# Kernel optimization log

Hardware: AMD Instinct MI355X
Metric: run time of the kernel (lower is better)

The kernel has to match this reference:

```python
import jax, jax.numpy as jnp
import numpy as np

HEADS = 12
HEAD_SIZE = 64
INF = 1e12  # K.infinity() in bert4keras

B, L, D = 8, 1024, 768


def setup_inputs() -> dict:
    key = jax.random.key(0)
    k1, k2 = jax.random.split(key)
    x = jax.random.normal(k1, (B, L, D), dtype=jnp.float32)
    W = jax.random.normal(k2, (D, HEADS * HEAD_SIZE * 2), dtype=jnp.float32) * (1.0 / np.sqrt(D))
    b = jnp.zeros((HEADS * HEAD_SIZE * 2,), dtype=jnp.float32)
    mask = jnp.ones((B, L), dtype=jnp.int32)
    return {"x": x, "W": W, "b": b, "mask": mask}


def _rope_sin_cos(seq_len, head_size, dtype):
    # SinusoidalPositionEmbedding(head_size, 'zero'):
    # emb[n, 2i] = sin(n * 10000^(-2i/S)), emb[n, 2i+1] = cos(...)
    pos = jnp.arange(seq_len, dtype=dtype)                       # [L]
    inv = jnp.power(jnp.asarray(10000.0, dtype),
                    -2.0 * jnp.arange(head_size // 2, dtype=dtype) / head_size)  # [S/2]
    ang = pos[:, None] * inv[None, :]                            # [L, S/2]
    # repeat_elements(..., 2, -1): [c0,c0,c1,c1,...]
    cos_pos = jnp.repeat(jnp.cos(ang), 2, axis=-1)               # [L, S]
    sin_pos = jnp.repeat(jnp.sin(ang), 2, axis=-1)               # [L, S]
    return sin_pos[None, :, None, :], cos_pos[None, :, None, :]  # [1,L,1,S]


def _rotate_half_interleaved(t):
    # stack([-t[...,1::2], t[...,::2]], -1).reshape(t.shape)
    t2 = jnp.stack([-t[..., 1::2], t[..., ::2]], axis=-1)
    return t2.reshape(t.shape)


def reference(x, W, b, mask):
    dtype = x.dtype
    Bq, Lq, _ = x.shape
    S = HEAD_SIZE
    # dense projection + head split: [B, L, H, 2S]
    proj = (jnp.einsum('bld,de->ble', x, W) + b).reshape(Bq, Lq, HEADS, 2 * S)
    qw, kw = proj[..., :S], proj[..., S:]
    # inline RoPE (interleaved variant)
    sin_pos, cos_pos = _rope_sin_cos(Lq, S, dtype)
    qw = qw * cos_pos + _rotate_half_interleaved(qw) * sin_pos
    kw = kw * cos_pos + _rotate_half_interleaved(kw) * sin_pos
    # bilinear score: [B, H, L, L]
    logits = jnp.einsum('bmhd,bnhd->bhmn', qw, kw)
    # padding mask on axis 2 (rows) and axis 3 (cols): x*m + (-INF)*(1-m)
    m = mask.astype(dtype)
    m_row = m[:, None, :, None]
    m_col = m[:, None, None, :]
    logits = logits * m_row + (-INF) * (1.0 - m_row)
    logits = logits * m_col + (-INF) * (1.0 - m_col)
    # upper-triangular (incl. diagonal) mask
    tri = jnp.triu(jnp.ones((Lq, Lq), dtype=dtype))
    logits = logits - (1.0 - tri) * INF
    return logits / np.sqrt(S).astype(np.float32)
```

## Files before the change

### kernel.cpp

```cpp
#include <hip/hip_runtime.h>
#include <hip/hip_bf16.h>
#include <stdint.h>

#define NHEADS 12
#define HS 64
#define NB 8
#define NL 1024
#define ND 768
#define NE 1536
#define INFV 1000000000000.0f

typedef __bf16 bf16x8 __attribute__((ext_vector_type(8)));
typedef float f32x4 __attribute__((ext_vector_type(4)));

typedef __attribute__((address_space(1))) const unsigned int gas_uint;
typedef __attribute__((address_space(3))) unsigned int las_uint;
#define GLOAD_LDS16(g, l) __builtin_amdgcn_global_load_lds((gas_uint*)(g), (las_uint*)(l), 16, 0, 0)

__device__ __forceinline__ unsigned short f2bf(float f) {
  unsigned int u = __builtin_bit_cast(unsigned int, f);
  u += 0x7fffu + ((u >> 16) & 1u);
  return (unsigned short)(u >> 16);
}

__device__ __forceinline__ bf16x8 load_frag(const unsigned short* p) {
  uint4 v = *(const uint4*)p;
  return __builtin_bit_cast(bf16x8, v);
}

__global__ __launch_bounds__(256) void k_prep(
    const float* __restrict__ W,
    unsigned short* __restrict__ wt,
    float* __restrict__ cst) {
  const int blk = blockIdx.x;
  if (blk < 288) {
    __shared__ float tile[64][65];
    int te = blk % 24, td = blk / 24;
    int c = threadIdx.x & 63, r4 = threadIdx.x >> 6;
    #pragma unroll
    for (int rr = 0; rr < 16; rr++) {
      int row = rr * 4 + r4;
      tile[row][c] = W[(size_t)(td * 64 + row) * NE + te * 64 + c];
    }
    __syncthreads();
    #pragma unroll
    for (int rr = 0; rr < 16; rr++) {
      int row = rr * 4 + r4;
      wt[(size_t)(te * 64 + row) * ND + td * 64 + c] = f2bf(tile[c][row]);
    }
  } else {
    int t = (blk - 288) * 256 + threadIdx.x;
    int p = t >> 5, i = t & 31;
    float inv = powf(10000.0f, -(float)i / 32.0f);
    float sv, cv;
    sincosf((float)p * inv, &sv, &cv);
    cst[(p * 32 + i) * 2 + 0] = cv;
    cst[(p * 32 + i) * 2 + 1] = sv;
  }
}

__global__ __launch_bounds__(256) void k_proj_rope(
    const float* __restrict__ x,
    const unsigned short* __restrict__ wt,
    const float* __restrict__ bias,
    const float* __restrict__ cst,
    unsigned short* __restrict__ qbuf, unsigned short* __restrict__ kbuf) {
  const int blk = blockIdx.x;
  const int xcd = blk & 7;
  const int loc = blk >> 3;
  const int h   = loc % 12;
  const int mt  = xcd * 8 + loc / 12;
  const int m0  = mt * 128;
  const int e0  = h * 128;
  const int tid  = threadIdx.x;
  const int lane = tid & 63;
  const int w    = tid >> 6;
  const int wm = w >> 1, wn = w & 1;
  const int col_l = lane & 15, rq = lane >> 4;

  __shared__ char smem_b[49152];

  unsigned int goffA[4];
  #pragma unroll
  for (int q = 0; q < 4; q++) {
    int p = q * 256 + tid;
    int r = p >> 3, sl = p & 7;
    goffA[q] = r * ND + (sl ^ (r & 7)) * 8;
  }
  unsigned int goffB[8];
  #pragma unroll
  for (int q = 0; q < 8; q++) {
    int p = q * 256 + tid;
    int r = p >> 4, sl = p & 15;
    goffB[q] = r * ND + (sl ^ (r & 15)) * 4;
  }
  const unsigned short* gA = wt + (size_t)e0 * ND;
  const float*          gB = x  + (size_t)m0 * ND;

  const int xr = col_l & 7;
  const unsigned int aRow = (unsigned)((wn * 64 + col_l) * 128);
  const unsigned int bRow = (unsigned)(16384 + (wm * 64 + col_l) * 256);

  f32x4 acc[4][4];
  #pragma unroll
  for (int i = 0; i < 4; i++)
    #pragma unroll
    for (int j = 0; j < 4; j++)
      #pragma unroll
      for (int q = 0; q < 4; q++) acc[i][j][q] = 0.0f;

  for (int kk = 0; kk < ND; kk += 64) {
    const unsigned short* sA = gA + kk;
    const float*          sB = gB + kk;
    #pragma unroll
    for (int q = 0; q < 4; q++) GLOAD_LDS16(sA + goffA[q], smem_b + (q * 256 + tid) * 16);
    #pragma unroll
    for (int q = 0; q < 8; q++) GLOAD_LDS16(sB + goffB[q], smem_b + 16384 + (q * 256 + tid) * 16);
    __syncthreads();
    #pragma unroll
    for (int kkh = 0; kkh < 2; kkh++) {
      bf16x8 af[4], bfr[4];
      #pragma unroll
      for (int f = 0; f < 4; f++) {
        af[f] = __builtin_bit_cast(bf16x8,
            *(const uint4*)(smem_b + aRow + f * 2048 + (((kkh << 2) | rq) ^ xr) * 16));
        const int sl0 = (kkh << 3) | (rq << 1);
        float4 lo = *(const float4*)(smem_b + bRow + f * 4096 + ((sl0 ^ col_l) * 16));
        float4 hi = *(const float4*)(smem_b + bRow + f * 4096 + (((sl0 + 1) ^ col_l) * 16));
        bfr[f] = bf16x8{(__bf16)lo.x, (__bf16)lo.y, (__bf16)lo.z, (__bf16)lo.w,
                        (__bf16)hi.x, (__bf16)hi.y, (__bf16)hi.z, (__bf16)hi.w};
      }
      #pragma unroll
      for (int i = 0; i < 4; i++)
        #pragma unroll
        for (int j = 0; j < 4; j++)
          acc[i][j] = __builtin_amdgcn_mfma_f32_16x16x32_bf16(af[i], bfr[j], acc[i][j], 0, 0, 0);
    }
    __syncthreads();
  }

  unsigned short* obuf = (wn == 1) ? kbuf : qbuf;
  #pragma unroll
  for (int j = 0; j < 4; j++) {
    const int m   = m0 + wm * 64 + j * 16 + col_l;
    const int pos = m & (NL - 1);
    const int bb  = m >> 10;
    const float* crow = cst + pos * 64;
    unsigned short* orow = obuf + (((size_t)(bb * NHEADS + h)) * NL + pos) * HS;
    #pragma unroll
    for (int i = 0; i < 4; i++) {
      const int s0 = i * 16 + rq * 4;
      float4 bv = *(const float4*)&bias[e0 + wn * 64 + s0];
      float4 tq = *(const float4*)(crow + s0);
      float v0 = acc[i][j][0] + bv.x;
      float v1 = acc[i][j][1] + bv.y;
      float v2 = acc[i][j][2] + bv.z;
      float v3 = acc[i][j][3] + bv.w;
      ushort4 o;
      o.x = f2bf(v0 * tq.x - v1 * tq.y);
      o.y = f2bf(v1 * tq.x + v0 * tq.y);
      o.z = f2bf(v2 * tq.z - v3 * tq.w);
      o.w = f2bf(v3 * tq.z + v2 * tq.w);
      *(ushort4*)&orow[s0] = o;
    }
  }
}

__global__ __launch_bounds__(256) void k_logits(
    const unsigned short* __restrict__ qbuf,
    const unsigned short* __restrict__ kbuf,
    const int* __restrict__ mask,
    float* __restrict__ out) {
  const int f  = blockIdx.x;
  const int r  = f & 7, t = f >> 3;
  const int bh = r + 8 * (t >> 6);
  const int tile = t & 63;
  const int tm = tile >> 3, tn = tile & 7;
  const int b  = bh / NHEADS;
  const int tid  = threadIdx.x;
  const int* mrow = mask + b * NL;

  if (tn < tm) {
    const int n0 = tn * 128 + (tid & 31) * 4;
    int4 mc = *(const int4*)&mrow[n0];
    #pragma unroll
    for (int it = 0; it < 16; it++) {
      int m = tm * 128 + it * 8 + (tid >> 5);
      float mr = (float)mrow[m];
      float base = -INFV * (1.0f - mr);
      f32x4 o;
      o[0] = ((mc.x ? base : -INFV) - INFV) * 0.125f;
      o[1] = ((mc.y ? base : -INFV) - INFV) * 0.125f;
      o[2] = ((mc.z ? base : -INFV) - INFV) * 0.125f;
      o[3] = ((mc.w ? base : -INFV) - INFV) * 0.125f;
      __builtin_nontemporal_store(o, (f32x4*)(out + ((size_t)bh * NL + m) * NL + n0));
    }
    return;
  }

  const int lane = tid & 63;
  const int w    = tid >> 6;
  const int wm = w >> 1, wn = w & 1;
  const int m_base = tm * 128 + wm * 64;
  const int n_base = tn * 128 + wn * 64;
  const int col_l = lane & 15, rq = lane >> 4;
  const unsigned short* Q = qbuf + (size_t)bh * (NL * HS);
  const unsigned short* K = kbuf + (size_t)bh * (NL * HS);

  __shared__ float lds[64 * 132];

  f32x4 acc[4][4];
  #pragma unroll
  for (int i = 0; i < 4; i++)
    #pragma unroll
    for (int j = 0; j < 4; j++)
      #pragma unroll
      for (int q = 0; q < 4; q++) acc[i][j][q] = 0.0f;

  #pragma unroll
  for (int ks = 0; ks < 2; ks++) {
    bf16x8 ak[4], bq[4];
    #pragma unroll
    for (int ff = 0; ff < 4; ff++) {
      ak[ff] = load_frag(K + (size_t)(n_base + ff * 16 + col_l) * HS + ks * 32 + rq * 8);
      bq[ff] = load_frag(Q + (size_t)(m_base + ff * 16 + col_l) * HS + ks * 32 + rq * 8);
    }
    #pragma unroll
    for (int i = 0; i < 4; i++)
      #pragma unroll
      for (int j = 0; j < 4; j++)
        acc[i][j] = __builtin_amdgcn_mfma_f32_16x16x32_bf16(ak[i], bq[j], acc[i][j], 0, 0, 0);
  }

  const bool diag = (tn == tm);
  const int rb_row = tid >> 5;
  const int rb_c4  = (tid & 31) * 4;
  const int n_rb   = tn * 128 + rb_c4;
  int4 mc_rb = *(const int4*)&mrow[n_rb];
  const bool allmc = (mc_rb.x & mc_rb.y & mc_rb.z & mc_rb.w) != 0;

  #pragma unroll
  for (int pass = 0; pass < 2; pass++) {
    if (wm == pass) {
      #pragma unroll
      for (int j = 0; j < 4; j++) {
        const int rl = j * 16 + col_l;
        #pragma unroll
        for (int i = 0; i < 4; i++)
          *(f32x4*)&lds[rl * 132 + wn * 64 + i * 16 + rq * 4] = acc[i][j];
      }
    }
    __syncthreads();
    #pragma unroll
    for (int it = 0; it < 8; it++) {
      const int rl = it * 8 + rb_row;
      const int m  = tm * 128 + pass * 64 + rl;
      f32x4 v = *(const f32x4*)&lds[rl * 132 + rb_c4];
      if (mrow[m] == 0) { v[0] = -INFV; v[1] = -INFV; v[2] = -INFV; v[3] = -INFV; }
      if (!allmc) {
        if (mc_rb.x == 0) v[0] = -INFV;
        if (mc_rb.y == 0) v[1] = -INFV;
        if (mc_rb.z == 0) v[2] = -INFV;
        if (mc_rb.w == 0) v[3] = -INFV;
      }
      if (diag) {
        if (n_rb + 0 < m) v[0] -= INFV;
        if (n_rb + 1 < m) v[1] -= INFV;
        if (n_rb + 2 < m) v[2] -= INFV;
        if (n_rb + 3 < m) v[3] -= INFV;
      }
      v *= 0.125f;
      __builtin_nontemporal_store(v, (f32x4*)(out + ((size_t)bh * NL + m) * NL + n_rb));
    }
    __syncthreads();
  }
}

extern "C" void kernel_launch(void* const* d_in, const int* in_sizes, int n_in,
                              void* d_out, int out_size, void* d_ws, size_t ws_size,
                              hipStream_t stream) {
  const float* x    = (const float*)d_in[0];
  const float* W    = (const float*)d_in[1];
  const float* bias = (const float*)d_in[2];
  const int*   mask = (const int*)d_in[3];
  float* out = (float*)d_out;
  char* ws = (char*)d_ws;

  unsigned short* wt = (unsigned short*)(ws);
  unsigned short* qb = (unsigned short*)(ws + 2359296);
  unsigned short* kb = (unsigned short*)(ws + 14942208);
  float* cst = (float*)(ws + 27525120);

  k_prep<<<416, 256, 0, stream>>>(W, wt, cst);
  k_proj_rope<<<768, 256, 0, stream>>>(x, wt, bias, cst, qb, kb);
  k_logits<<<6144, 256, 0, stream>>>(qb, kb, mask, out);
}
```

Baseline: 129.5 us.

## Move masked lower-triangle constant fill into projection GEMM main loop

The constant-fill work for lower-triangle tiles (below the diagonal, where the output is a mask constant) is moved out of the logits kernel and interleaved into the K-loop of the projection kernel. Each of the 768 projection blocks writes a slice of those tiles between iterations. The logits kernel now launches only the 36 upper-triangle tiles per (batch, head). The aim is to hide the large store-bound fill behind the compute-bound projection GEMM, at the cost of extra integer index math and store traffic inside the GEMM loop.

```diff
diff --git a/kernel.cpp b/kernel.cpp
--- a/kernel.cpp
+++ b/kernel.cpp
@@ -26,6 +26,32 @@
 __device__ __forceinline__ bf16x8 load_frag(const unsigned short* p) {
   uint4 v = *(const uint4*)p;
   return __builtin_bit_cast(bf16x8, v);
+}
+
+__device__ __forceinline__ void do_fill(int idx, const int* __restrict__ mask,
+                                        float* __restrict__ out) {
+  int t   = idx >> 12;
+  int w   = idx & 4095;
+  int row = w >> 5, cg = w & 31;
+  int bh  = t / 28;
+  int t28 = t - bh * 28;
+  float ft = sqrtf(8.0f * (float)t28 + 1.0f);
+  int tm = (int)((1.0f + ft) * 0.5f);
+  if (t28 < ((tm * (tm - 1)) >> 1)) tm--;
+  else if (t28 >= ((tm * (tm + 1)) >> 1)) tm++;
+  int tn = t28 - ((tm * (tm - 1)) >> 1);
+  int b  = bh / NHEADS;
+  int m  = tm * 128 + row;
+  const int* mrow = mask + b * NL;
+  float mr = (float)mrow[m];
+  int4 mc  = *(const int4*)&mrow[tn * 128 + cg * 4];
+  float base = -INFV * (1.0f - mr);
+  f32x4 o;
+  o[0] = ((mc.x ? base : -INFV) - INFV) * 0.125f;
+  o[1] = ((mc.y ? base : -INFV) - INFV) * 0.125f;
+  o[2] = ((mc.z ? base : -INFV) - INFV) * 0.125f;
+  o[3] = ((mc.w ? base : -INFV) - INFV) * 0.125f;
+  __builtin_nontemporal_store(o, (f32x4*)(out + ((size_t)bh * NL + m) * NL + tn * 128 + cg * 4));
 }
 
 __global__ __launch_bounds__(256) void k_prep(
@@ -64,7 +90,8 @@
     const unsigned short* __restrict__ wt,
     const float* __restrict__ bias,
     const float* __restrict__ cst,
-    unsigned short* __restrict__ qbuf, unsigned short* __restrict__ kbuf) {
+    unsigned short* __restrict__ qbuf, unsigned short* __restrict__ kbuf,
+    const int* __restrict__ mask, float* __restrict__ out) {
   const int blk = blockIdx.x;
   const int xcd = blk & 7;
   const int loc = blk >> 3;
@@ -77,6 +104,7 @@
   const int w    = tid >> 6;
   const int wm = w >> 1, wn = w & 1;
   const int col_l = lane & 15, rq = lane >> 4;
+  const int fill_base = blk * 14336 + tid;
 
   __shared__ char smem_b[49152];
 
@@ -109,7 +137,8 @@
       #pragma unroll
       for (int q = 0; q < 4; q++) acc[i][j][q] = 0.0f;
 
-  for (int kk = 0; kk < ND; kk += 64) {
+  int step = 0;
+  for (int kk = 0; kk < ND; kk += 64, step++) {
     const unsigned short* sA = gA + kk;
     const float*          sB = gB + kk;
     #pragma unroll
@@ -117,6 +146,11 @@
     #pragma unroll
     for (int q = 0; q < 8; q++) GLOAD_LDS16(sB + goffB[q], smem_b + 16384 + (q * 256 + tid) * 16);
     __syncthreads();
+    {
+      const int nst = (step < 8) ? 5 : 4;
+      const int sb  = (step < 8) ? step * 5 : 40 + (step - 8) * 4;
+      for (int q = 0; q < nst; q++) do_fill(fill_base + (sb + q) * 256, mask, out);
+    }
     #pragma unroll
     for (int kkh = 0; kkh < 2; kkh++) {
       bf16x8 af[4], bfr[4];
@@ -173,30 +207,15 @@
     float* __restrict__ out) {
   const int f  = blockIdx.x;
   const int r  = f & 7, t = f >> 3;
-  const int bh = r + 8 * (t >> 6);
-  const int tile = t & 63;
-  const int tm = tile >> 3, tn = tile & 7;
+  const int bh = r + 8 * (t / 36);
+  int u = t % 36;
+  int tm = 0;
+  #pragma unroll
+  for (int k = 0; k < 7; k++) if (u >= 8 - tm) { u -= 8 - tm; tm++; }
+  const int tn = tm + u;
   const int b  = bh / NHEADS;
   const int tid  = threadIdx.x;
   const int* mrow = mask + b * NL;
-
-  if (tn < tm) {
-    const int n0 = tn * 128 + (tid & 31) * 4;
-    int4 mc = *(const int4*)&mrow[n0];
-    #pragma unroll
-    for (int it = 0; it < 16; it++) {
-      int m = tm * 128 + it * 8 + (tid >> 5);
-      float mr = (float)mrow[m];
-      float base = -INFV * (1.0f - mr);
-      f32x4 o;
-      o[0] = ((mc.x ? base : -INFV) - INFV) * 0.125f;
-      o[1] = ((mc.y ? base : -INFV) - INFV) * 0.125f;
-      o[2] = ((mc.z ? base : -INFV) - INFV) * 0.125f;
-      o[3] = ((mc.w ? base : -INFV) - INFV) * 0.125f;
-      __builtin_nontemporal_store(o, (f32x4*)(out + ((size_t)bh * NL + m) * NL + n0));
-    }
-    return;
-  }
 
   const int lane = tid & 63;
   const int w    = tid >> 6;
@@ -292,6 +311,6 @@
   float* cst = (float*)(ws + 27525120);
 
   k_prep<<<416, 256, 0, stream>>>(W, wt, cst);
-  k_proj_rope<<<768, 256, 0, stream>>>(x, wt, bias, cst, qb, kb);
-  k_logits<<<6144, 256, 0, stream>>>(qb, kb, mask, out);
-}
+  k_proj_rope<<<768, 256, 0, stream>>>(x, wt, bias, cst, qb, kb, mask, out);
+  k_logits<<<3456, 256, 0, stream>>>(qb, kb, mask, out);
+}
```

Result: faster. 127.0 us (-2.0%).

## Move below-diagonal constant tile fills into projection kernel launch

Applied to the files above, without the earlier changes.

The strictly-lower-triangular output tiles, which only hold constant mask values, are now written by extra blocks appended to the projection kernel instead of by early-exit blocks in the logits kernel. The logits grid shrinks to only the upper-triangular tiles, and the tile index is decoded from a triangular enumeration. The aim is to overlap the roughly half-of-output store traffic with the compute-bound projection GEMM and to cut wasted block launches in the logits kernel. The cost is more blocks in the projection launch, which compete with it for bandwidth and compute units.

```diff
diff --git a/kernel.cpp b/kernel.cpp
--- a/kernel.cpp
+++ b/kernel.cpp
@@ -59,12 +59,46 @@
   }
 }
 
-__global__ __launch_bounds__(256) void k_proj_rope(
+__global__ __launch_bounds__(256) void k_proj_fill(
     const float* __restrict__ x,
     const unsigned short* __restrict__ wt,
     const float* __restrict__ bias,
     const float* __restrict__ cst,
-    unsigned short* __restrict__ qbuf, unsigned short* __restrict__ kbuf) {
+    unsigned short* __restrict__ qbuf, unsigned short* __restrict__ kbuf,
+    const int* __restrict__ mask, float* __restrict__ out) {
+  const int tid = threadIdx.x;
+
+  if (blockIdx.x >= 768) {
+    const int e   = blockIdx.x - 768;
+    const int bh  = e / 28;
+    int u = e % 28;
+    int tm = 1;
+    #pragma unroll
+    for (int k = 0; k < 6; k++) if (u >= tm) { u -= tm; tm++; }
+    const int tn = u;
+    const int b  = bh / NHEADS;
+    const int* mrow = mask + b * NL;
+    const int n0 = tn * 128 + (tid & 31) * 4;
+    int4 mc = *(const int4*)&mrow[n0];
+    float o0 = ((mc.x ? 0.0f : -INFV) - INFV) * 0.125f;
+    float o1 = ((mc.y ? 0.0f : -INFV) - INFV) * 0.125f;
+    float o2 = ((mc.z ? 0.0f : -INFV) - INFV) * 0.125f;
+    float o3 = ((mc.w ? 0.0f : -INFV) - INFV) * 0.125f;
+    const float oz = (-2.0f * INFV) * 0.125f;
+    #pragma unroll
+    for (int it = 0; it < 16; it++) {
+      int m = tm * 128 + it * 8 + (tid >> 5);
+      bool mr1 = (mrow[m] != 0);
+      f32x4 o;
+      o[0] = mr1 ? o0 : oz;
+      o[1] = mr1 ? o1 : oz;
+      o[2] = mr1 ? o2 : oz;
+      o[3] = mr1 ? o3 : oz;
+      __builtin_nontemporal_store(o, (f32x4*)(out + ((size_t)bh * NL + m) * NL + n0));
+    }
+    return;
+  }
+
   const int blk = blockIdx.x;
   const int xcd = blk & 7;
   const int loc = blk >> 3;
@@ -72,7 +106,6 @@
   const int mt  = xcd * 8 + loc / 12;
   const int m0  = mt * 128;
   const int e0  = h * 128;
-  const int tid  = threadIdx.x;
   const int lane = tid & 63;
   const int w    = tid >> 6;
   const int wm = w >> 1, wn = w & 1;
@@ -173,30 +206,15 @@
     float* __restrict__ out) {
   const int f  = blockIdx.x;
   const int r  = f & 7, t = f >> 3;
-  const int bh = r + 8 * (t >> 6);
-  const int tile = t & 63;
-  const int tm = tile >> 3, tn = tile & 7;
+  const int bh = r + 8 * (t / 36);
+  int u = t % 36;
+  int tm = 0;
+  #pragma unroll
+  for (int k = 0; k < 7; k++) if (u >= 8 - tm) { u -= 8 - tm; tm++; }
+  const int tn = tm + u;
   const int b  = bh / NHEADS;
   const int tid  = threadIdx.x;
   const int* mrow = mask + b * NL;
-
-  if (tn < tm) {
-    const int n0 = tn * 128 + (tid & 31) * 4;
-    int4 mc = *(const int4*)&mrow[n0];
-    #pragma unroll
-    for (int it = 0; it < 16; it++) {
-      int m = tm * 128 + it * 8 + (tid >> 5);
-      float mr = (float)mrow[m];
-      float base = -INFV * (1.0f - mr);
-      f32x4 o;
-      o[0] = ((mc.x ? base : -INFV) - INFV) * 0.125f;
-      o[1] = ((mc.y ? base : -INFV) - INFV) * 0.125f;
-      o[2] = ((mc.z ? base : -INFV) - INFV) * 0.125f;
-      o[3] = ((mc.w ? base : -INFV) - INFV) * 0.125f;
-      __builtin_nontemporal_store(o, (f32x4*)(out + ((size_t)bh * NL + m) * NL + n0));
-    }
-    return;
-  }
 
   const int lane = tid & 63;
   const int w    = tid >> 6;
@@ -292,6 +310,6 @@
   float* cst = (float*)(ws + 27525120);
 
   k_prep<<<416, 256, 0, stream>>>(W, wt, cst);
-  k_proj_rope<<<768, 256, 0, stream>>>(x, wt, bias, cst, qb, kb);
-  k_logits<<<6144, 256, 0, stream>>>(qb, kb, mask, out);
-}
+  k_proj_fill<<<768 + 2688, 256, 0, stream>>>(x, wt, bias, cst, qb, kb, mask, out);
+  k_logits<<<3456, 256, 0, stream>>>(qb, kb, mask, out);
+}
```

Result: no change. 127.6 us (-1.5%).
